# Kernel optimization log

Hardware: AMD Instinct MI355X
Metric: run time of the kernel (lower is better)

Reference implementation:

```python
import jax, jax.numpy as jnp
import numpy as np

EPS = 1e-12  # F.normalize eps

def _l2norm(x):
    n = jnp.linalg.norm(x, axis=-1, keepdims=True)
    return x / jnp.maximum(n, EPS)

def setup_inputs() -> dict:
    key = jax.random.key(0)
    k1, k2, k3, k4 = jax.random.split(key, 4)
    N, D = 16384, 256
    img = jax.random.normal(k1, (N, D), dtype=jnp.float32)
    txt = jax.random.normal(k2, (N, D), dtype=jnp.float32)
    t_prime = jax.random.normal(k3, (), dtype=jnp.float32)
    bias = jax.random.normal(k4, (), dtype=jnp.float32)
    return {"img": img, "txt": txt, "t_prime": t_prime, "bias": bias}

def reference(img, txt, t_prime, bias):
    # world_size == 1 path of DistributedSigLoss.forward
    n = img.shape[0]
    image_features = _l2norm(img)
    text_features = _l2norm(txt)
    # logits = exp(t') * img @ txt.T + b   -> [N, N]
    logits = jnp.exp(t_prime) * (image_features @ text_features.T) + bias
    # labels = 2*I - 1 (positive pairs on the diagonal, negatives elsewhere)
    labels = 2.0 * jnp.eye(n, dtype=logits.dtype) - 1.0
    loss = -jnp.sum(jax.nn.log_sigmoid(labels * logits)) / n
    return loss
```

## Files before the change

kernel.cpp:

```cpp
#include <hip/hip_runtime.h>

typedef int   i32x4 __attribute__((ext_vector_type(4)));
typedef int   i32x8 __attribute__((ext_vector_type(8)));
typedef float f32x16 __attribute__((ext_vector_type(16)));

#define D_DIM 256
#define LOG2E 1.4426950408889634f
#define LN2   0.6931471805599453f
#define STRIP_BYTES 32768
#define NBLK 16384
#define NPART (NBLK * 4)

#if __has_builtin(__builtin_amdgcn_exp2f)
static __device__ __forceinline__ float exp2_fast(float x) { return __builtin_amdgcn_exp2f(x); }
#else
static __device__ __forceinline__ float exp2_fast(float x) { return __expf(x * LN2); }
#endif
#if __has_builtin(__builtin_amdgcn_logf)
static __device__ __forceinline__ float log2_fast(float x) { return __builtin_amdgcn_logf(x); }
#else
static __device__ __forceinline__ float log2_fast(float x) { return __logf(x) * LOG2E; }
#endif

#if __has_builtin(__builtin_amdgcn_cvt_pk_fp8_f32)
static __device__ __forceinline__ unsigned int pack4_fp8(float a, float b, float c, float d) {
    int v = 0;
    v = __builtin_amdgcn_cvt_pk_fp8_f32(a, b, v, false);
    v = __builtin_amdgcn_cvt_pk_fp8_f32(c, d, v, true);
    return (unsigned int)v;
}
#else
#include <hip/hip_fp8.h>
static __device__ __forceinline__ unsigned char cv1(float x) {
    __hip_fp8_e4m3 f(x);
    union { __hip_fp8_e4m3 f; unsigned char b; } u; u.f = f; return u.b;
}
static __device__ __forceinline__ unsigned int pack4_fp8(float a, float b, float c, float d) {
    return (unsigned int)cv1(a) | ((unsigned int)cv1(b) << 8) |
           ((unsigned int)cv1(c) << 16) | ((unsigned int)cv1(d) << 24);
}
#endif

static __device__ __forceinline__ f32x16 mfma_fp8_32x32_k64(i32x8 a, i32x8 b, f32x16 c) {
#if __has_builtin(__builtin_amdgcn_mfma_scale_f32_32x32x64_f8f6f4)
    return __builtin_amdgcn_mfma_scale_f32_32x32x64_f8f6f4(a, b, c, 0, 0, 0, 127, 0, 127);
#else
    union { i32x8 v; long l[4]; } ua, ub;
    ua.v = a; ub.v = b;
#pragma unroll
    for (int s = 0; s < 4; ++s)
        c = __builtin_amdgcn_mfma_f32_32x32x16_fp8_fp8(ua.l[s], ub.l[s], c, 0, 0, 0);
    return c;
#endif
}

__global__ __launch_bounds__(256) void norm_cast_kernel(
    const float* __restrict__ img, const float* __restrict__ txt,
    unsigned char* __restrict__ Ab, unsigned char* __restrict__ Bb, int N)
{
    const int tid = threadIdx.x;
    const int q   = tid & 3;
    const int rl  = tid >> 2;
    int gRow = blockIdx.x * 64 + rl;

    const float* src;
    unsigned char* dstB;
    int row;
    if (gRow < N) { row = gRow;     src = img + (size_t)row * D_DIM; dstB = Ab; }
    else          { row = gRow - N; src = txt + (size_t)row * D_DIM; dstB = Bb; }

    float f[64];
    float ss = 0.0f;
    const float4* s4 = (const float4*)(src + q * 64);
#pragma unroll
    for (int i = 0; i < 16; ++i) {
        float4 v = s4[i];
        f[4*i+0] = v.x; f[4*i+1] = v.y; f[4*i+2] = v.z; f[4*i+3] = v.w;
        ss += v.x*v.x + v.y*v.y + v.z*v.z + v.w*v.w;
    }
    ss += __shfl_xor(ss, 1, 64);
    ss += __shfl_xor(ss, 2, 64);
    float inv = 1.0f / fmaxf(sqrtf(ss), 1e-12f);

    unsigned char* dst = dstB + (size_t)(row >> 7) * STRIP_BYTES + (row & 127) * 16;
#pragma unroll
    for (int g = 0; g < 4; ++g) {
        const float* h = f + g * 16;
        uint4 w;
        w.x = pack4_fp8(h[ 0]*inv, h[ 1]*inv, h[ 2]*inv, h[ 3]*inv);
        w.y = pack4_fp8(h[ 4]*inv, h[ 5]*inv, h[ 6]*inv, h[ 7]*inv);
        w.z = pack4_fp8(h[ 8]*inv, h[ 9]*inv, h[10]*inv, h[11]*inv);
        w.w = pack4_fp8(h[12]*inv, h[13]*inv, h[14]*inv, h[15]*inv);
        *(uint4*)(dst + (q * 4 + g) * 2048) = w;
    }
}

__global__ __launch_bounds__(256, 5) void siglip_loss_kernel(
    const unsigned char* __restrict__ A, const unsigned char* __restrict__ B,
    const float* __restrict__ t_prime, const float* __restrict__ bias,
    float* __restrict__ partials, int N)
{
    __shared__ unsigned char As[2][8192];
    __shared__ unsigned char Bs[2][8192];

    const int tid  = threadIdx.x;
    const int wave = tid >> 6;
    const int lane = tid & 63;
    const int r31  = lane & 31;
    const int g    = lane >> 5;
    const int wv   = wave >> 1;
    const int wu   = wave & 1;

    const int bid = blockIdx.x;
    const int st  = bid >> 8;
    const int l2  = bid & 255;
    const int bx  = (st & 7) * 16 + (l2 & 15);
    const int by  = (st >> 3) * 16 + (l2 >> 4);
    const int rowBase = by * 128;
    const int colBase = bx * 128;

    const unsigned char* Astrip = A + (size_t)by * STRIP_BYTES;
    const unsigned char* Bstrip = B + (size_t)bx * STRIP_BYTES;

    auto stage = [&](int buf, int c) {
        const unsigned char* ga = Astrip + c * 8192;
        const unsigned char* gb = Bstrip + c * 8192;
#pragma unroll
        for (int l = 0; l < 2; ++l) {
            int idx = wave * 2 + l;
            __builtin_amdgcn_global_load_lds(
                (const __attribute__((address_space(1))) unsigned int*)(ga + idx * 1024 + lane * 16),
                (__attribute__((address_space(3))) unsigned int*)&As[buf][idx * 1024],
                16, 0, 0);
            __builtin_amdgcn_global_load_lds(
                (const __attribute__((address_space(1))) unsigned int*)(gb + idx * 1024 + lane * 16),
                (__attribute__((address_space(3))) unsigned int*)&Bs[buf][idx * 1024],
                16, 0, 0);
        }
    };

    stage(0, 0);

    int a_off[2], b_off[2];
#pragma unroll
    for (int i = 0; i < 2; ++i) a_off[i] = g * 4096 + (wv * 64 + i * 32 + r31) * 16;
#pragma unroll
    for (int j = 0; j < 2; ++j) b_off[j] = g * 4096 + (wu * 64 + j * 32 + r31) * 16;

    f32x16 acc[2][2] = {};
    union F { i32x8 v8; i32x4 v4[2]; };

#pragma unroll 1
    for (int c = 0; c < 4; ++c) {
        __syncthreads();
        if (c < 3) stage((c + 1) & 1, c + 1);

        const unsigned char* as = As[c & 1];
        const unsigned char* bs = Bs[c & 1];
        F a[2], b[2];
#pragma unroll
        for (int i = 0; i < 2; ++i) {
            a[i].v4[0] = *(const i32x4*)&as[a_off[i]];
            a[i].v4[1] = *(const i32x4*)&as[a_off[i] + 2048];
            b[i].v4[0] = *(const i32x4*)&bs[b_off[i]];
            b[i].v4[1] = *(const i32x4*)&bs[b_off[i] + 2048];
        }
#pragma unroll
        for (int i = 0; i < 2; ++i)
#pragma unroll
            for (int j = 0; j < 2; ++j)
                acc[i][j] = mfma_fp8_32x32_k64(a[i].v8, b[j].v8, acc[i][j]);
    }

    const float s2 = __expf(t_prime[0]) * LOG2E;
    const float b2 = bias[0] * LOG2E;
    float local = 0.0f;
#pragma unroll
    for (int i = 0; i < 2; ++i)
#pragma unroll
        for (int j = 0; j < 2; ++j)
#pragma unroll
            for (int g2 = 0; g2 < 2; ++g2) {
                float x[8];
#pragma unroll
                for (int e = 0; e < 8; ++e)
                    x[e] = exp2_fast(fmaf(s2, acc[i][j][g2 * 8 + e], b2));
                float p = 1.0f + x[0];
#pragma unroll
                for (int e = 1; e < 8; ++e)
                    p = fmaf(p, x[e], p);
                local += log2_fast(p);
            }

    if (rowBase == colBase) {
#pragma unroll
        for (int i = 0; i < 2; ++i)
#pragma unroll
            for (int j = 0; j < 2; ++j)
#pragma unroll
                for (int r = 0; r < 16; ++r) {
                    int rowf = (r & 3) + 8 * (r >> 2) + 4 * g;
                    int grow = wv * 64 + i * 32 + rowf;
                    int gcol = wu * 64 + j * 32 + r31;
                    if (grow == gcol) local -= fmaf(s2, acc[i][j][r], b2);
                }
    }

#pragma unroll
    for (int off = 32; off > 0; off >>= 1)
        local += __shfl_xor(local, off, 64);
    if (lane == 0)
        partials[bid * 4 + wave] = local;
}

__global__ __launch_bounds__(1024) void reduce_kernel(
    const float* __restrict__ partials, float* __restrict__ out, int N)
{
    __shared__ float red[16];
    const int tid  = threadIdx.x;
    const int wave = tid >> 6;
    const int lane = tid & 63;
    float s = 0.0f;
#pragma unroll 4
    for (int i = tid; i < NPART; i += 1024)
        s += partials[i];
#pragma unroll
    for (int off = 32; off > 0; off >>= 1)
        s += __shfl_xor(s, off, 64);
    if (lane == 0) red[wave] = s;
    __syncthreads();
    if (tid == 0) {
        float t = 0.0f;
#pragma unroll
        for (int w = 0; w < 16; ++w) t += red[w];
        out[0] = t * (LN2 / (float)N);
    }
}

extern "C" void kernel_launch(void* const* d_in, const int* in_sizes, int n_in,
                              void* d_out, int out_size, void* d_ws, size_t ws_size,
                              hipStream_t stream) {
    const float* img = (const float*)d_in[0];
    const float* txt = (const float*)d_in[1];
    const float* tp  = (const float*)d_in[2];
    const float* bs  = (const float*)d_in[3];
    float* out = (float*)d_out;
    int N = in_sizes[0] / D_DIM;

    unsigned char* Ab = (unsigned char*)d_ws;
    unsigned char* Bb = Ab + (size_t)N * D_DIM;
    float* partials   = (float*)(Bb + (size_t)N * D_DIM);

    norm_cast_kernel<<<(2 * N) / 64, 256, 0, stream>>>(img, txt, Ab, Bb, N);
    siglip_loss_kernel<<<NBLK, 256, 0, stream>>>(Ab, Bb, tp, bs, partials, N);
    reduce_kernel<<<1, 1024, 0, stream>>>(partials, out, N);
}
```

Baseline: 182.9 us.

## Coalesce norm-cast reads per wave and stage fp8 output through swizzled LDS

```diff
diff --git a/kernel.cpp b/kernel.cpp
--- a/kernel.cpp
+++ b/kernel.cpp
@@ -58,44 +58,48 @@
     const float* __restrict__ img, const float* __restrict__ txt,
     unsigned char* __restrict__ Ab, unsigned char* __restrict__ Bb, int N)
 {
-    const int tid = threadIdx.x;
-    const int q   = tid & 3;
-    const int rl  = tid >> 2;
-    int gRow = blockIdx.x * 64 + rl;
-
-    const float* src;
-    unsigned char* dstB;
-    int row;
-    if (gRow < N) { row = gRow;     src = img + (size_t)row * D_DIM; dstB = Ab; }
-    else          { row = gRow - N; src = txt + (size_t)row * D_DIM; dstB = Bb; }
-
-    float f[64];
-    float ss = 0.0f;
-    const float4* s4 = (const float4*)(src + q * 64);
-#pragma unroll
-    for (int i = 0; i < 16; ++i) {
-        float4 v = s4[i];
-        f[4*i+0] = v.x; f[4*i+1] = v.y; f[4*i+2] = v.z; f[4*i+3] = v.w;
-        ss += v.x*v.x + v.y*v.y + v.z*v.z + v.w*v.w;
-    }
-    ss += __shfl_xor(ss, 1, 64);
-    ss += __shfl_xor(ss, 2, 64);
-    float inv = 1.0f / fmaxf(sqrtf(ss), 1e-12f);
-
-    unsigned char* dst = dstB + (size_t)(row >> 7) * STRIP_BYTES + (row & 127) * 16;
-#pragma unroll
-    for (int g = 0; g < 4; ++g) {
-        const float* h = f + g * 16;
-        uint4 w;
-        w.x = pack4_fp8(h[ 0]*inv, h[ 1]*inv, h[ 2]*inv, h[ 3]*inv);
-        w.y = pack4_fp8(h[ 4]*inv, h[ 5]*inv, h[ 6]*inv, h[ 7]*inv);
-        w.z = pack4_fp8(h[ 8]*inv, h[ 9]*inv, h[10]*inv, h[11]*inv);
-        w.w = pack4_fp8(h[12]*inv, h[13]*inv, h[14]*inv, h[15]*inv);
-        *(uint4*)(dst + (q * 4 + g) * 2048) = w;
-    }
-}
-
-__global__ __launch_bounds__(256, 5) void siglip_loss_kernel(
+    __shared__ unsigned char S[64 * 256];
+    const int tid  = threadIdx.x;
+    const int wave = tid >> 6;
+    const int lane = tid & 63;
+
+    int gRow0 = blockIdx.x * 64;
+    const float* srcM;
+    unsigned char* dstM;
+    int base;
+    if (gRow0 < N) { srcM = img; dstM = Ab; base = gRow0; }
+    else           { srcM = txt; dstM = Bb; base = gRow0 - N; }
+
+#pragma unroll
+    for (int p = 0; p < 16; ++p) {
+        int rl = p * 4 + wave;
+        float4 v = ((const float4*)(srcM + (size_t)(base + rl) * D_DIM))[lane];
+        float ss = v.x * v.x + v.y * v.y + v.z * v.z + v.w * v.w;
+#pragma unroll
+        for (int off = 32; off > 0; off >>= 1)
+            ss += __shfl_xor(ss, off, 64);
+        float inv = 1.0f / fmaxf(sqrtf(ss), 1e-12f);
+        unsigned int w4 = pack4_fp8(v.x * inv, v.y * inv, v.z * inv, v.w * inv);
+        int kc   = lane >> 2;
+        int phys = kc ^ (rl & 15);
+        *(unsigned int*)&S[rl * 256 + phys * 16 + (lane & 3) * 4] = w4;
+    }
+    __syncthreads();
+
+    int strip   = base >> 7;
+    int rowHalf = base & 127;
+    unsigned char* dstStrip = dstM + (size_t)strip * STRIP_BYTES;
+#pragma unroll
+    for (int q = 0; q < 4; ++q) {
+        int lin = q * 4096 + tid * 16;
+        int kc  = lin >> 10;
+        int rl  = (lin >> 4) & 63;
+        uint4 w = *(const uint4*)&S[rl * 256 + (kc ^ (rl & 15)) * 16];
+        *(uint4*)(dstStrip + kc * 2048 + (rowHalf + rl) * 16) = w;
+    }
+}
+
+__global__ __launch_bounds__(256, 4) void siglip_loss_kernel(
     const unsigned char* __restrict__ A, const unsigned char* __restrict__ B,
     const float* __restrict__ t_prime, const float* __restrict__ bias,
     float* __restrict__ partials, int N)
```

Result: faster. 168.1 us (-8.1%).
